# Performance work log

Measured on AMD Instinct MI355X. Metric: run time of the kernel, lower is better.

The kernel has to match this reference:

```python
import math
import jax, jax.numpy as jnp
import numpy as np

DIM = 2048
N_HEADS = 16
HEAD_DIM = DIM // N_HEADS
HID = 5632  # multiple_of*ceil(int(2*(4*dim)/3)/multiple_of)
EPS = 1e-5
B, S = 2, 2048


def setup_inputs() -> dict:
    key = jax.random.key(0)
    ks = jax.random.split(key, 12)
    sd = 0.02
    return {
        "x": jax.random.normal(ks[0], (B, S, DIM), jnp.float32),
        "mask": jnp.zeros((1, 1, S, S), jnp.float32),
        "attn_bias": jax.random.normal(ks[1], (1, N_HEADS, S, S), jnp.float32) * 0.1,
        "wq": jax.random.normal(ks[2], (DIM, DIM), jnp.float32) * sd,
        "wk": jax.random.normal(ks[3], (DIM, DIM), jnp.float32) * sd,
        "wv": jax.random.normal(ks[4], (DIM, DIM), jnp.float32) * sd,
        "wo": jax.random.normal(ks[5], (DIM, DIM), jnp.float32) * sd,
        "w1": jax.random.normal(ks[6], (HID, DIM), jnp.float32) * sd,
        "w2": jax.random.normal(ks[7], (DIM, HID), jnp.float32) * sd,
        "w3": jax.random.normal(ks[8], (HID, DIM), jnp.float32) * sd,
        "attn_norm_w": jnp.ones((DIM,), jnp.float32),
        "ffn_norm_w": jnp.ones((DIM,), jnp.float32),
    }


def rmsnorm(x, w):
    x32 = x.astype(jnp.float32)
    y = x32 * jax.lax.rsqrt(jnp.mean(x32 * x32, axis=-1, keepdims=True) + EPS)
    return y.astype(x.dtype) * w


def reference(x, mask, attn_bias, wq, wk, wv, wo, w1, w2, w3, attn_norm_w, ffn_norm_w):
    b, s, _ = x.shape
    # --- attention ---
    h = rmsnorm(x, attn_norm_w)
    q = (h @ wq.T).reshape(b, s, N_HEADS, HEAD_DIM)
    k = (h @ wk.T).reshape(b, s, N_HEADS, HEAD_DIM)
    v = (h @ wv.T).reshape(b, s, N_HEADS, HEAD_DIM)
    scores = jnp.einsum("bqhd,bkhd->bhqk", q, k) / math.sqrt(HEAD_DIM)
    scores = scores + attn_bias + mask
    probs = jax.nn.softmax(scores.astype(jnp.float32), axis=-1).astype(q.dtype)
    out = jnp.einsum("bhqk,bkhd->bqhd", probs, v).reshape(b, s, DIM)
    h1 = x + out @ wo.T
    # --- SwiGLU FFN ---
    f = rmsnorm(h1, ffn_norm_w)
    ff = (jax.nn.silu(f @ w1.T) * (f @ w3.T)) @ w2.T
    return h1 + ff
```

## Files before the change

kernel.cpp:

```cpp
#include <hip/hip_runtime.h>
#include <stdint.h>

typedef uint16_t u16;
typedef __attribute__((ext_vector_type(8))) short s16x8;
typedef __attribute__((ext_vector_type(4))) float f32x4;

typedef const __attribute__((address_space(1))) void* gptr_t;
typedef __attribute__((address_space(3))) void* lptr_t;

__device__ __forceinline__ float bf2f(u16 u) { return __uint_as_float(((unsigned)u) << 16); }
__device__ __forceinline__ u16 f2bf(float f) {
    unsigned u = __float_as_uint(f);
    u += 0x7fffu + ((u >> 16) & 1u);
    return (u16)(u >> 16);
}
__device__ __forceinline__ void gld_lds16(const void* g, void* l) {
    __builtin_amdgcn_global_load_lds((gptr_t)g, (lptr_t)l, 16, 0, 0);
}

__global__ __launch_bounds__(256) void cvt_f32_bf16(const float* __restrict__ src,
                                                    u16* __restrict__ dst, long n)
{
    const long i = ((long)blockIdx.x * 256 + threadIdx.x) * 8;
    if (i >= n) return;
    float4 a = *(const float4*)(src + i);
    float4 b = *(const float4*)(src + i + 4);
    u16 o8[8] = { f2bf(a.x), f2bf(a.y), f2bf(a.z), f2bf(a.w),
                  f2bf(b.x), f2bf(b.y), f2bf(b.z), f2bf(b.w) };
    *(uint4*)(dst + i) = *(const uint4*)o8;
}

__global__ __launch_bounds__(512, 2) void gemm256(
        const u16* __restrict__ A, const u16* __restrict__ B,
        u16* __restrict__ Cb, int M, int N, int K, int gx)
{
    __shared__ __align__(16) u16 As[2][256 * 64];
    __shared__ __align__(16) u16 Bs[2][256 * 64];

    const int tid  = threadIdx.x;
    const int wave = tid >> 6, lane = tid & 63;
    const int quad = lane >> 4, l16 = lane & 15;
    const int wmi = wave >> 2, wni = wave & 3;

    const int cpx = gridDim.x >> 3;
    const int wg  = ((int)blockIdx.x & 7) * cpx + ((int)blockIdx.x >> 3);
    const long m0 = (long)(wg / gx) * 256;
    const long n0 = (long)(wg % gx) * 256;

    f32x4 acc[8][4] = {};

    const u16* Ag = A + m0 * (long)K;
    const u16* Bg = B + n0 * (long)K;
    long soff[4];
    int  lbase[4];
#pragma unroll
    for (int i = 0; i < 4; i++) {
        const int c = i * 512 + tid;
        const int row = c >> 3, col8 = (c & 7) * 8;
        soff[i]  = (long)row * K + (col8 ^ ((row & 7) << 3));
        lbase[i] = (i * 512 + wave * 64) * 8;
    }

    const int T = K >> 6;

    auto issue = [&](int t, int slot) {
#pragma unroll
        for (int i = 0; i < 4; i++) {
            gld_lds16(Ag + soff[i] + (long)t * 64, &As[slot][lbase[i]]);
            gld_lds16(Bg + soff[i] + (long)t * 64, &Bs[slot][lbase[i]]);
        }
    };

    issue(0, 0);
    if (T > 1) issue(1, 1);

    const int swz   = (l16 & 7) << 3;
    const int arow0 = wmi * 128 + l16;
    const int brow0 = wni * 64 + l16;

    for (int t = 0; t < T; ++t) {
        const int slot = t & 1;
        if (t + 1 < T) {
            if (t >= 1) issue(t + 1, slot ^ 1);
            asm volatile("s_waitcnt vmcnt(8)" ::: "memory");
        } else {
            asm volatile("s_waitcnt vmcnt(0)" ::: "memory");
        }
        __builtin_amdgcn_sched_barrier(0);
        __builtin_amdgcn_s_barrier();
        __builtin_amdgcn_sched_barrier(0);

        s16x8 bfrag[4][2];
#pragma unroll
        for (int nt = 0; nt < 4; nt++)
#pragma unroll
            for (int kk = 0; kk < 2; kk++)
                bfrag[nt][kk] = *(const s16x8*)&Bs[slot][(brow0 + nt * 16) * 64
                                    + ((kk * 32 + quad * 8) ^ swz)];

#pragma unroll
        for (int p = 0; p < 4; p++) {
            s16x8 af[2][2];
#pragma unroll
            for (int mtl = 0; mtl < 2; mtl++)
#pragma unroll
                for (int kk = 0; kk < 2; kk++)
                    af[mtl][kk] = *(const s16x8*)&As[slot][(arow0 + (2 * p + mtl) * 16) * 64
                                        + ((kk * 32 + quad * 8) ^ swz)];
            __builtin_amdgcn_s_barrier();
            asm volatile("s_waitcnt lgkmcnt(0)" ::: "memory");
            __builtin_amdgcn_sched_barrier(0);
            __builtin_amdgcn_s_setprio(1);
#pragma unroll
            for (int mtl = 0; mtl < 2; mtl++)
#pragma unroll
                for (int nt = 0; nt < 4; nt++)
#pragma unroll
                    for (int kk = 0; kk < 2; kk++)
                        acc[2 * p + mtl][nt] = __builtin_amdgcn_mfma_f32_16x16x32_bf16(
                            af[mtl][kk], bfrag[nt][kk], acc[2 * p + mtl][nt], 0, 0, 0);
            __builtin_amdgcn_s_setprio(0);
            __builtin_amdgcn_s_barrier();
        }
    }

#pragma unroll
    for (int mt = 0; mt < 8; mt++)
#pragma unroll
        for (int nt = 0; nt < 4; nt++) {
            const long col = n0 + wni * 64 + nt * 16 + l16;
#pragma unroll
            for (int r = 0; r < 4; r++) {
                const long row = m0 + wmi * 128 + mt * 16 + quad * 4 + r;
                Cb[row * (long)N + col] = f2bf(acc[mt][nt][r]);
            }
        }
}

__global__ __launch_bounds__(256) void gemm_bt(
        const u16* __restrict__ A, const u16* __restrict__ B,
        u16* __restrict__ Cb, float* __restrict__ Cf, const float* __restrict__ Rf,
        int M, int N, int K, int lda, int ep)
{
    __shared__ __align__(16) u16 As[128 * 32];
    __shared__ __align__(16) u16 Bs[128 * 32];

    const int tid  = threadIdx.x;
    const int wave = tid >> 6, lane = tid & 63;
    const int quad = lane >> 4, l16 = lane & 15;
    const long m0 = (long)blockIdx.y * 128, n0 = (long)blockIdx.x * 128;
    const int wm = (wave >> 1) * 64, wn = (wave & 1) * 64;

    f32x4 acc[4][4] = {};

    const int c0 = tid, c1 = tid + 256;
    const u16* Ag = A + m0 * (long)lda;
    const u16* Bg = B + n0 * (long)K;
    const long aA0 = (long)(c0 >> 2) * lda + (c0 & 3) * 8;
    const long aA1 = (long)(c1 >> 2) * lda + (c1 & 3) * 8;
    const long aB0 = (long)(c0 >> 2) * K + (c0 & 3) * 8;
    const long aB1 = (long)(c1 >> 2) * K + (c1 & 3) * 8;
    const int lb0 = (wave * 64) * 8;
    const int lb1 = (256 + wave * 64) * 8;

    for (int k0 = 0; k0 < K; k0 += 32) {
        __syncthreads();
        gld_lds16(Ag + aA0 + k0, &As[lb0]);
        gld_lds16(Ag + aA1 + k0, &As[lb1]);
        gld_lds16(Bg + aB0 + k0, &Bs[lb0]);
        gld_lds16(Bg + aB1 + k0, &Bs[lb1]);
        __syncthreads();

        s16x8 af[4], bfr[4];
#pragma unroll
        for (int t = 0; t < 4; t++) {
            af[t]  = *(const s16x8*)&As[(wm + t * 16 + l16) * 32 + quad * 8];
            bfr[t] = *(const s16x8*)&Bs[(wn + t * 16 + l16) * 32 + quad * 8];
        }
#pragma unroll
        for (int mt = 0; mt < 4; mt++)
#pragma unroll
            for (int nt = 0; nt < 4; nt++)
                acc[mt][nt] = __builtin_amdgcn_mfma_f32_16x16x32_bf16(
                    af[mt], bfr[nt], acc[mt][nt], 0, 0, 0);
    }

#pragma unroll
    for (int mt = 0; mt < 4; mt++)
#pragma unroll
        for (int nt = 0; nt < 4; nt++) {
            const long col = n0 + wn + nt * 16 + l16;
#pragma unroll
            for (int r = 0; r < 4; r++) {
                const long row = m0 + wm + mt * 16 + quad * 4 + r;
                const long idx = row * N + col;
                const float v = acc[mt][nt][r];
                if (ep == 0) Cb[idx] = f2bf(v);
                else         Cf[idx] = v + Rf[idx];
            }
        }
}

__global__ __launch_bounds__(256) void flash_attn(
        const u16* __restrict__ Q, const u16* __restrict__ Kp,
        const u16* __restrict__ V, int ld, const float* __restrict__ bias,
        const float* __restrict__ mask, u16* __restrict__ O)
{
    const int tid  = threadIdx.x;
    const int wave = tid >> 6, lane = tid & 63;
    const int quad = lane >> 4, l16 = lane & 15;
    const int q0 = blockIdx.x * 64, h = blockIdx.y, b = blockIdx.z;

    __shared__ __align__(16) u16 Ks[64 * 128];
    __shared__ __align__(16) u16 Vt[128 * 64];
    __shared__ __align__(16) u16 Ps[4][16 * 64];

    const long baseI = (long)b * 2048 * ld + (long)h * 128;
    const long baseO = (long)b * 2048 * 2048 + (long)h * 128;

    s16x8 qf[4];
    {
        const u16* qp = Q + baseI + (long)(q0 + wave * 16 + l16) * ld;
#pragma unroll
        for (int kk = 0; kk < 4; kk++)
            qf[kk] = *(const s16x8*)(qp + kk * 32 + quad * 8);
    }

    f32x4 oacc[8] = {};
    float m_i[4] = { -1e30f, -1e30f, -1e30f, -1e30f };
    float l_i[4] = { 0.f, 0.f, 0.f, 0.f };
    const float scale = 0.08838834764831845f;
    const int kswz = (l16 & 7) << 3;

    for (int k0 = 0; k0 < 2048; k0 += 64) {
        __syncthreads();
#pragma unroll
        for (int it = 0; it < 4; it++) {
            const int c = it * 256 + tid;
            const int row = c >> 4, col8 = (c & 15) * 8;
            const int src = col8 ^ ((row & 7) << 3);
            gld_lds16(Kp + baseI + (long)(k0 + row) * ld + src,
                      &Ks[(it * 256 + wave * 64) * 8]);
        }
#pragma unroll
        for (int it = 0; it < 4; it++) {
            const int c = it * 256 + tid;
            const int row = c >> 4, col8 = (c & 15) * 8;
            uint4 raw = *(const uint4*)(V + baseI + (long)(k0 + row) * ld + col8);
            const u16* e = (const u16*)&raw;
#pragma unroll
            for (int j = 0; j < 8; j++) {
                const int d = col8 + j;
                const int swzv = ((d & 7) ^ ((d >> 3) & 7)) << 3;
                Vt[d * 64 + (row ^ swzv)] = e[j];
            }
        }
        __syncthreads();

        float sv[4][4];
#pragma unroll
        for (int nt = 0; nt < 4; nt++) {
            f32x4 sa = { 0.f, 0.f, 0.f, 0.f };
#pragma unroll
            for (int kk = 0; kk < 4; kk++) {
                s16x8 kf = *(const s16x8*)&Ks[(nt * 16 + l16) * 128
                                              + ((kk * 32 + quad * 8) ^ kswz)];
                sa = __builtin_amdgcn_mfma_f32_16x16x32_bf16(qf[kk], kf, sa, 0, 0, 0);
            }
            const int kcol = k0 + nt * 16 + l16;
#pragma unroll
            for (int r = 0; r < 4; r++) {
                const int qrow = q0 + wave * 16 + quad * 4 + r;
                float val = sa[r] * scale;
                val += bias[((long)h * 2048 + qrow) * 2048 + kcol];
                val += mask[(long)qrow * 2048 + kcol];
                sv[nt][r] = val;
            }
        }

        float alpha[4];
#pragma unroll
        for (int r = 0; r < 4; r++) {
            float mx = fmaxf(fmaxf(sv[0][r], sv[1][r]), fmaxf(sv[2][r], sv[3][r]));
#pragma unroll
            for (int off = 1; off < 16; off <<= 1) mx = fmaxf(mx, __shfl_xor(mx, off));
            const float mnew = fmaxf(m_i[r], mx);
            alpha[r] = __expf(m_i[r] - mnew);
            m_i[r] = mnew;
            float rs = 0.f;
#pragma unroll
            for (int nt = 0; nt < 4; nt++) {
                const float pv = __expf(sv[nt][r] - mnew);
                sv[nt][r] = pv;
                rs += pv;
            }
#pragma unroll
            for (int off = 1; off < 16; off <<= 1) rs += __shfl_xor(rs, off);
            l_i[r] = l_i[r] * alpha[r] + rs;
        }

#pragma unroll
        for (int nt = 0; nt < 4; nt++)
#pragma unroll
            for (int r = 0; r < 4; r++) {
                const int prow = quad * 4 + r;
                Ps[wave][prow * 64 + ((nt * 16 + l16) ^ ((prow & 7) << 3))]
                    = f2bf(sv[nt][r]);
            }

#pragma unroll
        for (int dt = 0; dt < 8; dt++)
#pragma unroll
            for (int r = 0; r < 4; r++)
                oacc[dt][r] *= alpha[r];

#pragma unroll
        for (int kk2 = 0; kk2 < 2; kk2++) {
            s16x8 pf = *(const s16x8*)&Ps[wave][l16 * 64
                                               + ((kk2 * 32 + quad * 8) ^ kswz)];
#pragma unroll
            for (int dt = 0; dt < 8; dt++) {
                const int d = dt * 16 + l16;
                const int vswz = ((d & 7) ^ ((d >> 3) & 7)) << 3;
                s16x8 vf = *(const s16x8*)&Vt[d * 64
                                              + ((kk2 * 32 + quad * 8) ^ vswz)];
                oacc[dt] = __builtin_amdgcn_mfma_f32_16x16x32_bf16(pf, vf, oacc[dt], 0, 0, 0);
            }
        }
    }

#pragma unroll
    for (int dt = 0; dt < 8; dt++)
#pragma unroll
        for (int r = 0; r < 4; r++) {
            const int qrow = q0 + wave * 16 + quad * 4 + r;
            O[baseO + (long)qrow * 2048 + dt * 16 + l16] = f2bf(oacc[dt][r] / l_i[r]);
        }
}

__global__ __launch_bounds__(256) void rmsnorm_f32(
        const float* __restrict__ x, const float* __restrict__ w,
        u16* __restrict__ out)
{
    const int row = blockIdx.x, tid = threadIdx.x;
    const float* xr = x + (long)row * 2048;
    float4 f0 = *(const float4*)(xr + tid * 8);
    float4 f1 = *(const float4*)(xr + tid * 8 + 4);
    float v[8] = { f0.x, f0.y, f0.z, f0.w, f1.x, f1.y, f1.z, f1.w };
    float ss = 0.f;
#pragma unroll
    for (int j = 0; j < 8; j++) ss += v[j] * v[j];
#pragma unroll
    for (int off = 32; off > 0; off >>= 1) ss += __shfl_xor(ss, off);
    __shared__ float red[4];
    if ((tid & 63) == 0) red[tid >> 6] = ss;
    __syncthreads();
    const float tot = red[0] + red[1] + red[2] + red[3];
    const float sc = rsqrtf(tot * (1.0f / 2048.0f) + 1e-5f);
    float4 w0 = *(const float4*)(w + tid * 8);
    float4 w1v = *(const float4*)(w + tid * 8 + 4);
    const float wv[8] = { w0.x, w0.y, w0.z, w0.w, w1v.x, w1v.y, w1v.z, w1v.w };
    u16 o8[8];
#pragma unroll
    for (int j = 0; j < 8; j++) o8[j] = f2bf(v[j] * sc * wv[j]);
    *(uint4*)(out + (long)row * 2048 + tid * 8) = *(const uint4*)o8;
}

__global__ __launch_bounds__(704) void silu_mul_rows(u16* __restrict__ s13)
{
    const long rb = (long)blockIdx.x * 11264;
    const int col8 = threadIdx.x * 8;
    uint4 ra = *(const uint4*)(s13 + rb + col8);
    uint4 rbv = *(const uint4*)(s13 + rb + 5632 + col8);
    const u16* ea = (const u16*)&ra;
    const u16* eb = (const u16*)&rbv;
    u16 o8[8];
#pragma unroll
    for (int j = 0; j < 8; j++) {
        const float fa = bf2f(ea[j]);
        const float fb = bf2f(eb[j]);
        const float s = fa / (1.f + __expf(-fa));
        o8[j] = f2bf(s * fb);
    }
    *(uint4*)(s13 + rb + col8) = *(const uint4*)o8;
}

extern "C" void kernel_launch(void* const* d_in, const int* in_sizes, int n_in,
                              void* d_out, int out_size, void* d_ws, size_t ws_size,
                              hipStream_t stream)
{
    const float* x    = (const float*)d_in[0];
    const float* mask = (const float*)d_in[1];
    const float* bias = (const float*)d_in[2];
    const float* wq   = (const float*)d_in[3];
    const float* wk   = (const float*)d_in[4];
    const float* wv   = (const float*)d_in[5];
    const float* wo   = (const float*)d_in[6];
    const float* w1   = (const float*)d_in[7];
    const float* w2   = (const float*)d_in[8];
    const float* w3   = (const float*)d_in[9];
    const float* anw  = (const float*)d_in[10];
    const float* fnw  = (const float*)d_in[11];
    float* out = (float*)d_out;

    const long SZA = 2048L * 2048;
    const long SZF = 5632L * 2048;

    char* p = (char*)d_ws;
    u16* wqb = (u16*)p;  u16* wkb = wqb + SZA;  u16* wvb = wkb + SZA;
    u16* wob = wvb + SZA;
    u16* w1b = wob + SZA;  u16* w3b = w1b + SZF;  u16* w2b = w3b + SZF;
    p += (4 * SZA + 3 * SZF) * 2;
    const size_t SZ = (size_t)4096 * 2048 * 2;
    u16* h_buf  = (u16*)p;  p += SZ;
    u16* qkv    = (u16*)p;  p += (size_t)4096 * 6144 * 2;
    u16* s13    = (u16*)p;  p += (size_t)4096 * 11264 * 2;

    cvt_f32_bf16<<<2048, 256, 0, stream>>>(wq, wqb, SZA);
    cvt_f32_bf16<<<2048, 256, 0, stream>>>(wk, wkb, SZA);
    cvt_f32_bf16<<<2048, 256, 0, stream>>>(wv, wvb, SZA);
    cvt_f32_bf16<<<2048, 256, 0, stream>>>(wo, wob, SZA);
    cvt_f32_bf16<<<5632, 256, 0, stream>>>(w1, w1b, SZF);
    cvt_f32_bf16<<<5632, 256, 0, stream>>>(w3, w3b, SZF);
    cvt_f32_bf16<<<5632, 256, 0, stream>>>(w2, w2b, SZF);

    rmsnorm_f32<<<4096, 256, 0, stream>>>(x, anw, h_buf);
    gemm256<<<384, 512, 0, stream>>>(h_buf, wqb, qkv, 4096, 6144, 2048, 24);
    flash_attn<<<dim3(32, 16, 2), 256, 0, stream>>>(qkv, qkv + 2048, qkv + 4096,
                                                    6144, bias, mask, h_buf);
    gemm_bt<<<dim3(16, 32), 256, 0, stream>>>(h_buf, wob, nullptr, out, x,
                                              4096, 2048, 2048, 2048, 1);
    rmsnorm_f32<<<4096, 256, 0, stream>>>(out, fnw, h_buf);
    gemm256<<<704, 512, 0, stream>>>(h_buf, w1b, s13, 4096, 11264, 2048, 44);
    silu_mul_rows<<<4096, 704, 0, stream>>>(s13);
    gemm_bt<<<dim3(16, 32), 256, 0, stream>>>(s13, w2b, nullptr, out, out,
                                              4096, 2048, 5632, 11264, 1);
}
```

Measured before the change: 1.437 ms.

## Template pipelined 256-row GEMM over tile width and epilogue; replace simple gemm_bt

Makes the double-buffered, swizzled 256x256 GEMM a template over N-tile width (128 or 256) and epilogue type (bf16 store or fp32 residual add), and adds a separate A leading dimension. The Wo and W2 projections, which used the simpler single-buffered 128x128 gemm_bt with K-step 32, now use the pipelined kernel with 256x128 tiles. The QKV GEMM moves to 256x128 tiles to double the block count and fill more CUs. Narrower tiles lower per-block arithmetic intensity, and the residual epilogue writes fp32 with scattered per-lane stores.

```diff
diff --git a/kernel.cpp b/kernel.cpp
--- a/kernel.cpp
+++ b/kernel.cpp
@@ -30,12 +30,16 @@
     *(uint4*)(dst + i) = *(const uint4*)o8;
 }
 
-__global__ __launch_bounds__(512, 2) void gemm256(
+template<int BN, int EP>
+__global__ __launch_bounds__(512, 2) void gemm256t(
         const u16* __restrict__ A, const u16* __restrict__ B,
-        u16* __restrict__ Cb, int M, int N, int K, int gx)
-{
+        u16* __restrict__ Cb, float* __restrict__ Cf, const float* __restrict__ Rf,
+        int M, int N, int K, int lda, int gx)
+{
+    constexpr int NB = BN / 64;
+    constexpr int NT = BN / 64;
     __shared__ __align__(16) u16 As[2][256 * 64];
-    __shared__ __align__(16) u16 Bs[2][256 * 64];
+    __shared__ __align__(16) u16 Bs[2][BN * 64];
 
     const int tid  = threadIdx.x;
     const int wave = tid >> 6, lane = tid & 63;
@@ -45,30 +49,38 @@
     const int cpx = gridDim.x >> 3;
     const int wg  = ((int)blockIdx.x & 7) * cpx + ((int)blockIdx.x >> 3);
     const long m0 = (long)(wg / gx) * 256;
-    const long n0 = (long)(wg % gx) * 256;
-
-    f32x4 acc[8][4] = {};
-
-    const u16* Ag = A + m0 * (long)K;
+    const long n0 = (long)(wg % gx) * BN;
+
+    f32x4 acc[8][NT] = {};
+
+    const u16* Ag = A + m0 * (long)lda;
     const u16* Bg = B + n0 * (long)K;
-    long soff[4];
-    int  lbase[4];
+    long soffA[4]; int lbA[4];
 #pragma unroll
     for (int i = 0; i < 4; i++) {
         const int c = i * 512 + tid;
         const int row = c >> 3, col8 = (c & 7) * 8;
-        soff[i]  = (long)row * K + (col8 ^ ((row & 7) << 3));
-        lbase[i] = (i * 512 + wave * 64) * 8;
+        soffA[i] = (long)row * lda + (col8 ^ ((row & 7) << 3));
+        lbA[i]   = (i * 512 + wave * 64) * 8;
+    }
+    long soffB[NB]; int lbB[NB];
+#pragma unroll
+    for (int i = 0; i < NB; i++) {
+        const int c = i * 512 + tid;
+        const int row = c >> 3, col8 = (c & 7) * 8;
+        soffB[i] = (long)row * K + (col8 ^ ((row & 7) << 3));
+        lbB[i]   = (i * 512 + wave * 64) * 8;
     }
 
     const int T = K >> 6;
 
     auto issue = [&](int t, int slot) {
 #pragma unroll
-        for (int i = 0; i < 4; i++) {
-            gld_lds16(Ag + soff[i] + (long)t * 64, &As[slot][lbase[i]]);
-            gld_lds16(Bg + soff[i] + (long)t * 64, &Bs[slot][lbase[i]]);
-        }
+        for (int i = 0; i < 4; i++)
+            gld_lds16(Ag + soffA[i] + (long)t * 64, &As[slot][lbA[i]]);
+#pragma unroll
+        for (int i = 0; i < NB; i++)
+            gld_lds16(Bg + soffB[i] + (long)t * 64, &Bs[slot][lbB[i]]);
     };
 
     issue(0, 0);
@@ -76,13 +88,16 @@
 
     const int swz   = (l16 & 7) << 3;
     const int arow0 = wmi * 128 + l16;
-    const int brow0 = wni * 64 + l16;
+    const int brow0 = wni * (BN / 4) + l16;
 
     for (int t = 0; t < T; ++t) {
         const int slot = t & 1;
         if (t + 1 < T) {
             if (t >= 1) issue(t + 1, slot ^ 1);
-            asm volatile("s_waitcnt vmcnt(8)" ::: "memory");
+            if constexpr (BN == 256)
+                asm volatile("s_waitcnt vmcnt(8)" ::: "memory");
+            else
+                asm volatile("s_waitcnt vmcnt(6)" ::: "memory");
         } else {
             asm volatile("s_waitcnt vmcnt(0)" ::: "memory");
         }
@@ -90,9 +105,9 @@
         __builtin_amdgcn_s_barrier();
         __builtin_amdgcn_sched_barrier(0);
 
-        s16x8 bfrag[4][2];
-#pragma unroll
-        for (int nt = 0; nt < 4; nt++)
+        s16x8 bfrag[NT][2];
+#pragma unroll
+        for (int nt = 0; nt < NT; nt++)
 #pragma unroll
             for (int kk = 0; kk < 2; kk++)
                 bfrag[nt][kk] = *(const s16x8*)&Bs[slot][(brow0 + nt * 16) * 64
@@ -114,7 +129,7 @@
 #pragma unroll
             for (int mtl = 0; mtl < 2; mtl++)
 #pragma unroll
-                for (int nt = 0; nt < 4; nt++)
+                for (int nt = 0; nt < NT; nt++)
 #pragma unroll
                     for (int kk = 0; kk < 2; kk++)
                         acc[2 * p + mtl][nt] = __builtin_amdgcn_mfma_f32_16x16x32_bf16(
@@ -127,76 +142,15 @@
 #pragma unroll
     for (int mt = 0; mt < 8; mt++)
 #pragma unroll
-        for (int nt = 0; nt < 4; nt++) {
-            const long col = n0 + wni * 64 + nt * 16 + l16;
+        for (int nt = 0; nt < NT; nt++) {
+            const long col = n0 + wni * (BN / 4) + nt * 16 + l16;
 #pragma unroll
             for (int r = 0; r < 4; r++) {
                 const long row = m0 + wmi * 128 + mt * 16 + quad * 4 + r;
-                Cb[row * (long)N + col] = f2bf(acc[mt][nt][r]);
-            }
-        }
-}
-
-__global__ __launch_bounds__(256) void gemm_bt(
-        const u16* __restrict__ A, const u16* __restrict__ B,
-        u16* __restrict__ Cb, float* __restrict__ Cf, const float* __restrict__ Rf,
-        int M, int N, int K, int lda, int ep)
-{
-    __shared__ __align__(16) u16 As[128 * 32];
-    __shared__ __align__(16) u16 Bs[128 * 32];
-
-    const int tid  = threadIdx.x;
-    const int wave = tid >> 6, lane = tid & 63;
-    const int quad = lane >> 4, l16 = lane & 15;
-    const long m0 = (long)blockIdx.y * 128, n0 = (long)blockIdx.x * 128;
-    const int wm = (wave >> 1) * 64, wn = (wave & 1) * 64;
-
-    f32x4 acc[4][4] = {};
-
-    const int c0 = tid, c1 = tid + 256;
-    const u16* Ag = A + m0 * (long)lda;
-    const u16* Bg = B + n0 * (long)K;
-    const long aA0 = (long)(c0 >> 2) * lda + (c0 & 3) * 8;
-    const long aA1 = (long)(c1 >> 2) * lda + (c1 & 3) * 8;
-    const long aB0 = (long)(c0 >> 2) * K + (c0 & 3) * 8;
-    const long aB1 = (long)(c1 >> 2) * K + (c1 & 3) * 8;
-    const int lb0 = (wave * 64) * 8;
-    const int lb1 = (256 + wave * 64) * 8;
-
-    for (int k0 = 0; k0 < K; k0 += 32) {
-        __syncthreads();
-        gld_lds16(Ag + aA0 + k0, &As[lb0]);
-        gld_lds16(Ag + aA1 + k0, &As[lb1]);
-        gld_lds16(Bg + aB0 + k0, &Bs[lb0]);
-        gld_lds16(Bg + aB1 + k0, &Bs[lb1]);
-        __syncthreads();
-
-        s16x8 af[4], bfr[4];
-#pragma unroll
-        for (int t = 0; t < 4; t++) {
-            af[t]  = *(const s16x8*)&As[(wm + t * 16 + l16) * 32 + quad * 8];
-            bfr[t] = *(const s16x8*)&Bs[(wn + t * 16 + l16) * 32 + quad * 8];
-        }
-#pragma unroll
-        for (int mt = 0; mt < 4; mt++)
-#pragma unroll
-            for (int nt = 0; nt < 4; nt++)
-                acc[mt][nt] = __builtin_amdgcn_mfma_f32_16x16x32_bf16(
-                    af[mt], bfr[nt], acc[mt][nt], 0, 0, 0);
-    }
-
-#pragma unroll
-    for (int mt = 0; mt < 4; mt++)
-#pragma unroll
-        for (int nt = 0; nt < 4; nt++) {
-            const long col = n0 + wn + nt * 16 + l16;
-#pragma unroll
-            for (int r = 0; r < 4; r++) {
-                const long row = m0 + wm + mt * 16 + quad * 4 + r;
-                const long idx = row * N + col;
+                const long idx = row * (long)N + col;
                 const float v = acc[mt][nt][r];
-                if (ep == 0) Cb[idx] = f2bf(v);
-                else         Cf[idx] = v + Rf[idx];
+                if constexpr (EP == 0) Cb[idx] = f2bf(v);
+                else                   Cf[idx] = v + Rf[idx];
             }
         }
 }
@@ -425,14 +379,16 @@
     cvt_f32_bf16<<<5632, 256, 0, stream>>>(w2, w2b, SZF);
 
     rmsnorm_f32<<<4096, 256, 0, stream>>>(x, anw, h_buf);
-    gemm256<<<384, 512, 0, stream>>>(h_buf, wqb, qkv, 4096, 6144, 2048, 24);
+    gemm256t<128, 0><<<768, 512, 0, stream>>>(h_buf, wqb, qkv, nullptr, nullptr,
+                                              4096, 6144, 2048, 2048, 48);
     flash_attn<<<dim3(32, 16, 2), 256, 0, stream>>>(qkv, qkv + 2048, qkv + 4096,
                                                     6144, bias, mask, h_buf);
-    gemm_bt<<<dim3(16, 32), 256, 0, stream>>>(h_buf, wob, nullptr, out, x,
-                                              4096, 2048, 2048, 2048, 1);
+    gemm256t<128, 1><<<256, 512, 0, stream>>>(h_buf, wob, nullptr, out, x,
+                                              4096, 2048, 2048, 2048, 16);
     rmsnorm_f32<<<4096, 256, 0, stream>>>(out, fnw, h_buf);
-    gemm256<<<704, 512, 0, stream>>>(h_buf, w1b, s13, 4096, 11264, 2048, 44);
+    gemm256t<256, 0><<<704, 512, 0, stream>>>(h_buf, w1b, s13, nullptr, nullptr,
+                                              4096, 11264, 2048, 2048, 44);
     silu_mul_rows<<<4096, 704, 0, stream>>>(s13);
-    gemm_bt<<<dim3(16, 32), 256, 0, stream>>>(s13, w2b, nullptr, out, out,
-                                              4096, 2048, 5632, 11264, 1);
-}
+    gemm256t<128, 1><<<256, 512, 0, stream>>>(s13, w2b, nullptr, out, out,
+                                              4096, 2048, 5632, 11264, 16);
+}
```

Measured after the change: 1.414 ms. About the same (-1.6%).
